# Optimization experiments

Measured on AMD Instinct MI355X. Metric: run time of the kernel, lower is better.

Reference implementation:

```python
import math
import jax, jax.numpy as jnp
import numpy as np

B, D, C = 1024, 512, 100000
S = 30.0
M = 0.3
COS_M = math.cos(M)
SIN_M = math.sin(M)
TH = math.cos(math.pi - M)
MM = math.sin(math.pi - M) * M
EPS = 1e-12  # torch F.normalize eps


def _l2norm(x):
    n = jnp.sqrt(jnp.sum(x * x, axis=-1, keepdims=True))
    return x / jnp.maximum(n, EPS)


def setup_inputs() -> dict:
    key = jax.random.key(0)
    k1, k2, k3 = jax.random.split(key, 3)
    features = jax.random.normal(k1, (B, D), dtype=jnp.float32)
    # xavier_uniform_ for weight [C, D]
    limit = math.sqrt(6.0 / (C + D))
    weight = jax.random.uniform(k2, (C, D), dtype=jnp.float32, minval=-limit, maxval=limit)
    targets = jax.random.randint(k3, (B,), 0, C, dtype=jnp.int64)
    return {"features": features, "weight": weight, "targets": targets}


def reference(features, weight, targets):
    # cosine similarity via normalized GEMM: [B, C]
    cosine = _l2norm(features) @ _l2norm(weight).T
    cosine = cosine.astype(jnp.float32)
    sine = jnp.sqrt(jnp.maximum(1.0 - cosine * cosine, 0.0))
    phi = cosine * COS_M - sine * SIN_M
    # easy_margin=False branch
    phi = jnp.where(cosine > TH, phi, cosine - MM)
    # one-hot blend (ls_eps == 0): target column gets phi, rest keep cosine
    one_hot = targets[:, None] == jnp.arange(C)[None, :]
    logits = jnp.where(one_hot, phi, cosine) * S
    # CrossEntropyLoss (mean reduction)
    logp = jax.nn.log_softmax(logits, axis=-1)
    loss = -jnp.mean(jnp.take_along_axis(logp, targets[:, None], axis=1))
    return loss
```

## Files before the change

### kernel.cpp

```cpp
#include <hip/hip_runtime.h>

#define B_ROWS 1024
#define D_DIM  512
#define C_CLS  100000
#define N_TILES 782
#define GRID_NJ 98

typedef unsigned short u16;
typedef __attribute__((ext_vector_type(8))) short bf16x8;
typedef __attribute__((ext_vector_type(4))) float f32x4;

__device__ __forceinline__ u16 f2bf(float f) {
  unsigned u = __float_as_uint(f);
  u += 0x7fffu + ((u >> 16) & 1u);
  return (u16)(u >> 16);
}

__device__ __forceinline__ bf16x8 pack8(float4 a, float4 b) {
  union { bf16x8 v; unsigned u[4]; } r;
  r.u[0] = __builtin_amdgcn_perm(__float_as_uint(a.y), __float_as_uint(a.x), 0x07060302u);
  r.u[1] = __builtin_amdgcn_perm(__float_as_uint(a.w), __float_as_uint(a.z), 0x07060302u);
  r.u[2] = __builtin_amdgcn_perm(__float_as_uint(b.y), __float_as_uint(b.x), 0x07060302u);
  r.u[3] = __builtin_amdgcn_perm(__float_as_uint(b.w), __float_as_uint(b.z), 0x07060302u);
  return r.v;
}

__device__ __forceinline__ void gll16(const void* g, void* l) {
  __builtin_amdgcn_global_load_lds(
      (const __attribute__((address_space(1))) unsigned int*)g,
      (__attribute__((address_space(3))) unsigned int*)l, 16, 0, 0);
}

__global__ void norm_feat_kernel(const float* __restrict__ in, u16* __restrict__ out)
{
  const int row  = blockIdx.x * 4 + (threadIdx.x >> 6);
  const int lane = threadIdx.x & 63;
  const float4* r = (const float4*)(in + (size_t)row * D_DIM);
  float4 v0 = r[lane];
  float4 v1 = r[lane + 64];
  float ss = v0.x*v0.x + v0.y*v0.y + v0.z*v0.z + v0.w*v0.w
           + v1.x*v1.x + v1.y*v1.y + v1.z*v1.z + v1.w*v1.w;
#pragma unroll
  for (int m = 1; m < 64; m <<= 1) ss += __shfl_xor(ss, m);
  const float inv = 1.0f / fmaxf(sqrtf(ss), 1e-12f);
  ushort4 o0, o1;
  o0.x = f2bf(v0.x * inv); o0.y = f2bf(v0.y * inv);
  o0.z = f2bf(v0.z * inv); o0.w = f2bf(v0.w * inv);
  o1.x = f2bf(v1.x * inv); o1.y = f2bf(v1.y * inv);
  o1.z = f2bf(v1.z * inv); o1.w = f2bf(v1.w * inv);
  ushort4* orow = (ushort4*)(out + (size_t)row * D_DIM);
  orow[lane]      = o0;
  orow[lane + 64] = o1;
}

__global__ __launch_bounds__(256, 4) void arc_gemm(
    const u16* __restrict__ fn, const float* __restrict__ wt,
    const int* __restrict__ targets, float* __restrict__ psum,
    float* __restrict__ tlogit)
{
  __shared__ u16 As[128 * 32];
  __shared__ u16 Ws[128 * 32];
  __shared__ int tg[128];
  __shared__ float winv[128];

  const int tid = threadIdx.x;
  const int bx  = blockIdx.x;
  const int xcd = bx & 7;
  const int l   = bx >> 3;
  const int tile_ni = (l >> 3) * 8 + xcd;
  if (tile_ni >= N_TILES) return;
  const int tile_m = (l & 7) << 7;
  const int tile_n = tile_ni << 7;

  if (tid < 128) tg[tid] = targets[tile_m + tid];

  const int wave = tid >> 6, lane = tid & 63;
  const int wm = wave >> 1, wno = wave & 1;
  const int quad = lane >> 4, l15 = lane & 15;

  f32x4 acc[4][4] = {};

  const int srow   = tid >> 2;
  const int schunk = (tid & 3) ^ ((tid >> 3) & 3);
  const u16* Ag = fn + (size_t)(tile_m + srow) * D_DIM + schunk * 8;
  u16* Asd0 = As + tid * 8;
  u16* Asd1 = As + 2048 + tid * 8;
  const int wr0 = tile_n + srow;
  const int wr1 = wr0 + 64;
  const float* Wg0 = wt + (size_t)min(wr0, C_CLS - 1) * D_DIM + schunk * 8;
  const float* Wg1 = wt + (size_t)min(wr1, C_CLS - 1) * D_DIM + schunk * 8;
  u16* Wsd0 = Ws + tid * 8;
  u16* Wsd1 = Ws + 2048 + tid * 8;

  const int rsw = (quad ^ ((l15 >> 1) & 3)) * 8;
  const u16* ApA = As + (wm * 64 + l15) * 32 + rsw;
  const u16* ApW = Ws + (wno * 64 + l15) * 32 + rsw;

  float ssq0 = 0.0f, ssq1 = 0.0f;

  for (int k0 = 0; k0 < D_DIM; k0 += 32) {
    const float4 wa = *(const float4*)(Wg0 + k0);
    const float4 wb = *(const float4*)(Wg0 + k0 + 4);
    const float4 wc = *(const float4*)(Wg1 + k0);
    const float4 wd = *(const float4*)(Wg1 + k0 + 4);
    gll16(Ag + k0, Asd0);
    gll16(Ag + 64 * D_DIM + k0, Asd1);
    ssq0 += wa.x*wa.x + wa.y*wa.y + wa.z*wa.z + wa.w*wa.w
          + wb.x*wb.x + wb.y*wb.y + wb.z*wb.z + wb.w*wb.w;
    ssq1 += wc.x*wc.x + wc.y*wc.y + wc.z*wc.z + wc.w*wc.w
          + wd.x*wd.x + wd.y*wd.y + wd.z*wd.z + wd.w*wd.w;
    *(bf16x8*)Wsd0 = pack8(wa, wb);
    *(bf16x8*)Wsd1 = pack8(wc, wd);
    __syncthreads();
    bf16x8 af[4], wf[4];
#pragma unroll
    for (int r = 0; r < 4; r++) af[r] = *(const bf16x8*)(ApA + r * 16 * 32);
#pragma unroll
    for (int r = 0; r < 4; r++) wf[r] = *(const bf16x8*)(ApW + r * 16 * 32);
#pragma unroll
    for (int rm = 0; rm < 4; rm++)
#pragma unroll
      for (int rn = 0; rn < 4; rn++)
        acc[rm][rn] = __builtin_amdgcn_mfma_f32_16x16x32_bf16(
            af[rm], wf[rn], acc[rm][rn], 0, 0, 0);
    __syncthreads();
  }

  ssq0 += __shfl_xor(ssq0, 1); ssq0 += __shfl_xor(ssq0, 2);
  ssq1 += __shfl_xor(ssq1, 1); ssq1 += __shfl_xor(ssq1, 2);
  if ((tid & 3) == 0) {
    winv[srow]      = 1.0f / fmaxf(sqrtf(ssq0), 1e-12f);
    winv[srow + 64] = 1.0f / fmaxf(sqrtf(ssq1), 1e-12f);
  }
  __syncthreads();

  float wiv[4];
#pragma unroll
  for (int rn = 0; rn < 4; rn++) wiv[rn] = winv[wno * 64 + rn * 16 + l15];

  const float Sc   = 30.0f;
  const float COSM = 0.9553364891256060f;
  const float SINM = 0.2955202066613396f;
  const float THc  = -0.9553364891256060f;
  const float MMc  = 0.0886560619984019f;

#pragma unroll
  for (int rm = 0; rm < 4; rm++) {
#pragma unroll
    for (int reg = 0; reg < 4; reg++) {
      const int bl = wm * 64 + rm * 16 + quad * 4 + reg;
      const int b = tile_m + bl;
      const int tgt = tg[bl];
      float s = 0.0f;
#pragma unroll
      for (int rn = 0; rn < 4; rn++) {
        const int c = tile_n + wno * 64 + rn * 16 + l15;
        const float cosv = acc[rm][rn][reg] * wiv[rn];
        float logit = Sc * cosv;
        if (c == tgt) {
          const float sine = sqrtf(fmaxf(1.0f - cosv * cosv, 0.0f));
          float phi = cosv * COSM - sine * SINM;
          phi = (cosv > THc) ? phi : (cosv - MMc);
          logit = Sc * phi;
          tlogit[b] = logit;
        }
        s += (c < C_CLS) ? __expf(logit - 30.0f) : 0.0f;
      }
      s += __shfl_xor(s, 1);
      s += __shfl_xor(s, 2);
      s += __shfl_xor(s, 4);
      s += __shfl_xor(s, 8);
      if (l15 == 0) atomicAdd(psum + b, s);
    }
  }
}

__global__ void finalize_loss(const float* __restrict__ psum,
                              const float* __restrict__ tlogit,
                              float* __restrict__ out)
{
  const int tid = threadIdx.x;
  float s = 0.0f;
  for (int i = tid; i < B_ROWS; i += 256)
    s += 30.0f + logf(psum[i]) - tlogit[i];
#pragma unroll
  for (int m = 1; m < 64; m <<= 1) s += __shfl_xor(s, m);
  __shared__ float red[4];
  if ((tid & 63) == 0) red[tid >> 6] = s;
  __syncthreads();
  if (tid == 0) out[0] = (red[0] + red[1] + red[2] + red[3]) * (1.0f / B_ROWS);
}

extern "C" void kernel_launch(void* const* d_in, const int* in_sizes, int n_in,
                              void* d_out, int out_size, void* d_ws, size_t ws_size,
                              hipStream_t stream) {
  const float* feat = (const float*)d_in[0];
  const float* wt   = (const float*)d_in[1];
  const int*   tgt  = (const int*)d_in[2];
  float* out = (float*)d_out;
  char* ws = (char*)d_ws;

  u16* fn = (u16*)ws;
  float* psum = (float*)(ws + (size_t)B_ROWS * D_DIM * 2);
  float* tlogit = psum + B_ROWS;

  hipMemsetAsync(psum, 0, B_ROWS * sizeof(float), stream);
  norm_feat_kernel<<<B_ROWS / 4, 256, 0, stream>>>(feat, fn);
  arc_gemm<<<GRID_NJ * 8 * 8, 256, 0, stream>>>(fn, wt, tgt, psum, tlogit);
  finalize_loss<<<1, 256, 0, stream>>>(psum, tlogit, out);
}
```

Baseline: 459.8 us.

## Pre-normalize weight to bf16 in a prep pass and stream it via LDS DMA

Adds a prep kernel that L2-normalizes both features and the weight matrix, writes them as bf16 into workspace, and zeroes psum, which replaces the memset. The GEMM then loads pre-normalized bf16 weight tiles with global_load_lds instead of reading fp32 weight, converting it, and computing row norms in every M-tile block. The raw fp32 weight is otherwise re-read by each of the 8 M-tiles, so this cuts GEMM traffic and ALU work. In exchange it adds a pass that reads the full fp32 weight once and writes a 100 MB bf16 copy. It falls back to the old path when the workspace is too small.

```diff
diff --git a/kernel.cpp b/kernel.cpp
--- a/kernel.cpp
+++ b/kernel.cpp
@@ -31,7 +31,138 @@
       (__attribute__((address_space(3))) unsigned int*)l, 16, 0, 0);
 }
 
-__global__ void norm_feat_kernel(const float* __restrict__ in, u16* __restrict__ out)
+__global__ void prep_kernel(const float* __restrict__ feat,
+                            const float* __restrict__ wt,
+                            u16* __restrict__ fn, u16* __restrict__ wb,
+                            float* __restrict__ psum)
+{
+  const int row  = blockIdx.x * 4 + (threadIdx.x >> 6);
+  const int lane = threadIdx.x & 63;
+  const float* src = (row < B_ROWS) ? feat + (size_t)row * D_DIM
+                                    : wt + (size_t)(row - B_ROWS) * D_DIM;
+  u16* dst = (row < B_ROWS) ? fn + (size_t)row * D_DIM
+                            : wb + (size_t)(row - B_ROWS) * D_DIM;
+  const float4* r = (const float4*)src;
+  float4 v0 = r[lane];
+  float4 v1 = r[lane + 64];
+  float ss = v0.x*v0.x + v0.y*v0.y + v0.z*v0.z + v0.w*v0.w
+           + v1.x*v1.x + v1.y*v1.y + v1.z*v1.z + v1.w*v1.w;
+#pragma unroll
+  for (int m = 1; m < 64; m <<= 1) ss += __shfl_xor(ss, m);
+  const float inv = 1.0f / fmaxf(sqrtf(ss), 1e-12f);
+  ushort4 o0, o1;
+  o0.x = f2bf(v0.x * inv); o0.y = f2bf(v0.y * inv);
+  o0.z = f2bf(v0.z * inv); o0.w = f2bf(v0.w * inv);
+  o1.x = f2bf(v1.x * inv); o1.y = f2bf(v1.y * inv);
+  o1.z = f2bf(v1.z * inv); o1.w = f2bf(v1.w * inv);
+  ushort4* od = (ushort4*)dst;
+  od[lane]      = o0;
+  od[lane + 64] = o1;
+  if (row < B_ROWS && lane == 0) psum[row] = 0.0f;
+}
+
+__global__ __launch_bounds__(256, 4) void arc_gemm_pre(
+    const u16* __restrict__ fn, const u16* __restrict__ wb,
+    const int* __restrict__ targets, float* __restrict__ psum,
+    float* __restrict__ tlogit)
+{
+  __shared__ u16 As[128 * 32];
+  __shared__ u16 Ws[128 * 32];
+  __shared__ int tg[128];
+
+  const int tid = threadIdx.x;
+  const int bx  = blockIdx.x;
+  const int xcd = bx & 7;
+  const int l   = bx >> 3;
+  const int tile_ni = (l >> 3) * 8 + xcd;
+  if (tile_ni >= N_TILES) return;
+  const int tile_m = (l & 7) << 7;
+  const int tile_n = tile_ni << 7;
+
+  if (tid < 128) tg[tid] = targets[tile_m + tid];
+
+  const int wave = tid >> 6, lane = tid & 63;
+  const int wm = wave >> 1, wno = wave & 1;
+  const int quad = lane >> 4, l15 = lane & 15;
+
+  f32x4 acc[4][4] = {};
+
+  const int srow   = tid >> 2;
+  const int schunk = (tid & 3) ^ ((tid >> 3) & 3);
+  const u16* Ag = fn + (size_t)(tile_m + srow) * D_DIM + schunk * 8;
+  const int wr0 = tile_n + srow;
+  const int wr1 = wr0 + 64;
+  const u16* Wg0 = wb + (size_t)min(wr0, C_CLS - 1) * D_DIM + schunk * 8;
+  const u16* Wg1 = wb + (size_t)min(wr1, C_CLS - 1) * D_DIM + schunk * 8;
+  u16* Asd0 = As + tid * 8;
+  u16* Asd1 = As + 2048 + tid * 8;
+  u16* Wsd0 = Ws + tid * 8;
+  u16* Wsd1 = Ws + 2048 + tid * 8;
+
+  const int rsw = (quad ^ ((l15 >> 1) & 3)) * 8;
+  const u16* ApA = As + (wm * 64 + l15) * 32 + rsw;
+  const u16* ApW = Ws + (wno * 64 + l15) * 32 + rsw;
+
+  for (int k0 = 0; k0 < D_DIM; k0 += 32) {
+    gll16(Ag + k0, Asd0);
+    gll16(Ag + 64 * D_DIM + k0, Asd1);
+    gll16(Wg0 + k0, Wsd0);
+    gll16(Wg1 + k0, Wsd1);
+    __syncthreads();
+    bf16x8 af[4], wf[4];
+#pragma unroll
+    for (int r = 0; r < 4; r++) af[r] = *(const bf16x8*)(ApA + r * 16 * 32);
+#pragma unroll
+    for (int r = 0; r < 4; r++) wf[r] = *(const bf16x8*)(ApW + r * 16 * 32);
+#pragma unroll
+    for (int rm = 0; rm < 4; rm++)
+#pragma unroll
+      for (int rn = 0; rn < 4; rn++)
+        acc[rm][rn] = __builtin_amdgcn_mfma_f32_16x16x32_bf16(
+            af[rm], wf[rn], acc[rm][rn], 0, 0, 0);
+    __syncthreads();
+  }
+
+  const float Sc   = 30.0f;
+  const float COSM = 0.9553364891256060f;
+  const float SINM = 0.2955202066613396f;
+  const float THc  = -0.9553364891256060f;
+  const float MMc  = 0.0886560619984019f;
+
+#pragma unroll
+  for (int rm = 0; rm < 4; rm++) {
+#pragma unroll
+    for (int reg = 0; reg < 4; reg++) {
+      const int bl = wm * 64 + rm * 16 + quad * 4 + reg;
+      const int b = tile_m + bl;
+      const int tgt = tg[bl];
+      float s = 0.0f;
+#pragma unroll
+      for (int rn = 0; rn < 4; rn++) {
+        const int c = tile_n + wno * 64 + rn * 16 + l15;
+        const float cosv = acc[rm][rn][reg];
+        float logit = Sc * cosv;
+        if (c == tgt) {
+          const float sine = sqrtf(fmaxf(1.0f - cosv * cosv, 0.0f));
+          float phi = cosv * COSM - sine * SINM;
+          phi = (cosv > THc) ? phi : (cosv - MMc);
+          logit = Sc * phi;
+          tlogit[b] = logit;
+        }
+        s += (c < C_CLS) ? __expf(logit - 30.0f) : 0.0f;
+      }
+      s += __shfl_xor(s, 1);
+      s += __shfl_xor(s, 2);
+      s += __shfl_xor(s, 4);
+      s += __shfl_xor(s, 8);
+      if (l15 == 0) atomicAdd(psum + b, s);
+    }
+  }
+}
+
+__global__ void norm_feat_kernel(const float* __restrict__ in,
+                                 u16* __restrict__ out,
+                                 float* __restrict__ psum)
 {
   const int row  = blockIdx.x * 4 + (threadIdx.x >> 6);
   const int lane = threadIdx.x & 63;
@@ -51,9 +182,10 @@
   ushort4* orow = (ushort4*)(out + (size_t)row * D_DIM);
   orow[lane]      = o0;
   orow[lane + 64] = o1;
-}
-
-__global__ __launch_bounds__(256, 4) void arc_gemm(
+  if (lane == 0) psum[row] = 0.0f;
+}
+
+__global__ __launch_bounds__(256, 4) void arc_gemm_raw(
     const u16* __restrict__ fn, const float* __restrict__ wt,
     const int* __restrict__ targets, float* __restrict__ psum,
     float* __restrict__ tlogit)
@@ -100,16 +232,16 @@
 
   for (int k0 = 0; k0 < D_DIM; k0 += 32) {
     const float4 wa = *(const float4*)(Wg0 + k0);
-    const float4 wb = *(const float4*)(Wg0 + k0 + 4);
+    const float4 wb2 = *(const float4*)(Wg0 + k0 + 4);
     const float4 wc = *(const float4*)(Wg1 + k0);
     const float4 wd = *(const float4*)(Wg1 + k0 + 4);
     gll16(Ag + k0, Asd0);
     gll16(Ag + 64 * D_DIM + k0, Asd1);
     ssq0 += wa.x*wa.x + wa.y*wa.y + wa.z*wa.z + wa.w*wa.w
-          + wb.x*wb.x + wb.y*wb.y + wb.z*wb.z + wb.w*wb.w;
+          + wb2.x*wb2.x + wb2.y*wb2.y + wb2.z*wb2.z + wb2.w*wb2.w;
     ssq1 += wc.x*wc.x + wc.y*wc.y + wc.z*wc.z + wc.w*wc.w
           + wd.x*wd.x + wd.y*wd.y + wd.z*wd.z + wd.w*wd.w;
-    *(bf16x8*)Wsd0 = pack8(wa, wb);
+    *(bf16x8*)Wsd0 = pack8(wa, wb2);
     *(bf16x8*)Wsd1 = pack8(wc, wd);
     __syncthreads();
     bf16x8 af[4], wf[4];
@@ -200,12 +332,24 @@
   float* out = (float*)d_out;
   char* ws = (char*)d_ws;
 
-  u16* fn = (u16*)ws;
-  float* psum = (float*)(ws + (size_t)B_ROWS * D_DIM * 2);
-  float* tlogit = psum + B_ROWS;
-
-  hipMemsetAsync(psum, 0, B_ROWS * sizeof(float), stream);
-  norm_feat_kernel<<<B_ROWS / 4, 256, 0, stream>>>(feat, fn);
-  arc_gemm<<<GRID_NJ * 8 * 8, 256, 0, stream>>>(fn, wt, tgt, psum, tlogit);
-  finalize_loss<<<1, 256, 0, stream>>>(psum, tlogit, out);
-}
+  const size_t fn_bytes = (size_t)B_ROWS * D_DIM * 2;
+  const size_t wb_bytes = (size_t)C_CLS * D_DIM * 2;
+  const size_t tail     = 2 * (size_t)B_ROWS * sizeof(float);
+
+  if (ws_size >= fn_bytes + wb_bytes + tail) {
+    u16* fn = (u16*)ws;
+    u16* wb = (u16*)(ws + fn_bytes);
+    float* psum = (float*)(ws + fn_bytes + wb_bytes);
+    float* tlogit = psum + B_ROWS;
+    prep_kernel<<<(B_ROWS + C_CLS) / 4, 256, 0, stream>>>(feat, wt, fn, wb, psum);
+    arc_gemm_pre<<<GRID_NJ * 8 * 8, 256, 0, stream>>>(fn, wb, tgt, psum, tlogit);
+    finalize_loss<<<1, 256, 0, stream>>>(psum, tlogit, out);
+  } else {
+    u16* fn = (u16*)ws;
+    float* psum = (float*)(ws + fn_bytes);
+    float* tlogit = psum + B_ROWS;
+    norm_feat_kernel<<<B_ROWS / 4, 256, 0, stream>>>(feat, fn, psum);
+    arc_gemm_raw<<<GRID_NJ * 8 * 8, 256, 0, stream>>>(fn, wt, tgt, psum, tlogit);
+    finalize_loss<<<1, 256, 0, stream>>>(psum, tlogit, out);
+  }
+}
```

Result: slower. 480.6 us (+4.5%).
